# Performance work log

Hardware: AMD Instinct MI355X
Metric: run time of the kernel (lower is better)

## Reference

```python
import jax, jax.numpy as jnp
import numpy as np

B, S, E, H, V = 32, 128, 512, 512, 32000


def setup_inputs() -> dict:
    key = jax.random.key(0)
    ks = jax.random.split(key, 8)
    s_ih = 1.0 / np.sqrt(H)
    return {
        "embed_x": jax.random.normal(ks[0], (B, S, E), dtype=jnp.float32),
        "hidden": jax.random.normal(ks[1], (1, B, H), dtype=jnp.float32),
        "w_ih": jax.random.uniform(ks[2], (3 * H, E), dtype=jnp.float32, minval=-s_ih, maxval=s_ih),
        "w_hh": jax.random.uniform(ks[3], (3 * H, H), dtype=jnp.float32, minval=-s_ih, maxval=s_ih),
        "b_ih": jax.random.uniform(ks[4], (3 * H,), dtype=jnp.float32, minval=-s_ih, maxval=s_ih),
        "b_hh": jax.random.uniform(ks[5], (3 * H,), dtype=jnp.float32, minval=-s_ih, maxval=s_ih),
        "w_out": jax.random.normal(ks[6], (V, H), dtype=jnp.float32) * (1.0 / np.sqrt(H)),
    }


def reference(embed_x, hidden, w_ih, w_hh, b_ih, b_hh, w_out):
    # Single-layer GRU (PyTorch gate order: r, z, n), batch_first, then a
    # per-step bias-free projection to vocab. Dropout p=0 -> identity.
    h0 = hidden[0]                                  # [B, H]
    hsz = h0.shape[-1]
    # Precompute input contribution for all timesteps: [S, B, 3H]
    x_gates = jnp.einsum('bse,ge->sbg', embed_x, w_ih) + b_ih

    def step(h, xg):
        hg = h @ w_hh.T + b_hh                      # [B, 3H]
        xr, xz, xn = jnp.split(xg, 3, axis=-1)
        hr, hz, hn = jnp.split(hg, 3, axis=-1)
        r = jax.nn.sigmoid(xr + hr)
        z = jax.nn.sigmoid(xz + hz)
        n = jnp.tanh(xn + r * hn)
        h_new = (1.0 - z) * n + z * h
        return h_new, h_new

    _, hs = jax.lax.scan(step, h0, x_gates)         # hs: [S, B, H]
    # Projection to vocab (bias-free): [B, S, V]
    logits = jnp.einsum('sbh,vh->bsv', hs, w_out)
    return logits
```

## Files before the change

### kernel.cpp

```cpp
#include <hip/hip_runtime.h>

typedef unsigned short ushort_t;
typedef unsigned int uint_t;
typedef __attribute__((ext_vector_type(4))) float f32x4;
typedef __attribute__((ext_vector_type(8))) __bf16 bf16x8;

constexpr int BB = 32, SS = 128, EE = 512, HH = 512, VV = 32000;
constexpr int MM = BB * SS;
constexpr int G3 = 3 * HH;
constexpr int SCAN_WG = 32;

__device__ inline ushort_t f2b(float f) {
  union { float f; uint_t u; } v; v.f = f;
  uint_t r = v.u + 0x7fffu + ((v.u >> 16) & 1u);
  return (ushort_t)(r >> 16);
}
__device__ inline float b2f(ushort_t u) {
  union { float f; uint_t u; } v; v.u = ((uint_t)u) << 16;
  return v.f;
}

__global__ void cvt_bf16(const float* __restrict__ s, ushort_t* __restrict__ d, int n4) {
  int i = blockIdx.x * blockDim.x + threadIdx.x;
  if (i >= n4) return;
  float4 v = reinterpret_cast<const float4*>(s)[i];
  ushort4 o;
  o.x = f2b(v.x); o.y = f2b(v.y); o.z = f2b(v.z); o.w = f2b(v.w);
  reinterpret_cast<ushort4*>(d)[i] = o;
}

__global__ void cvt_split(const float* __restrict__ s, ushort_t* __restrict__ hi,
                          ushort_t* __restrict__ lo, int n4) {
  int i = blockIdx.x * blockDim.x + threadIdx.x;
  if (i >= n4) return;
  float4 v = reinterpret_cast<const float4*>(s)[i];
  float a[4] = {v.x, v.y, v.z, v.w};
  ushort4 oh, ol;
  ushort_t h;
  h = f2b(a[0]); oh.x = h; ol.x = f2b(a[0] - b2f(h));
  h = f2b(a[1]); oh.y = h; ol.y = f2b(a[1] - b2f(h));
  h = f2b(a[2]); oh.z = h; ol.z = f2b(a[2] - b2f(h));
  h = f2b(a[3]); oh.w = h; ol.w = f2b(a[3] - b2f(h));
  reinterpret_cast<ushort4*>(hi)[i] = oh;
  reinterpret_cast<ushort4*>(lo)[i] = ol;
}

__global__ __launch_bounds__(256) void gemm_bt(
    const ushort_t* __restrict__ A, const ushort_t* __restrict__ B,
    float* __restrict__ C, const float* __restrict__ bias,
    int M, int N, int K) {
  __shared__ alignas(16) ushort_t As[128 * 32];
  __shared__ alignas(16) ushort_t Bs[128 * 32];
  const int tid = threadIdx.x;
  const int wave = tid >> 6, lane = tid & 63;
  const int l16 = lane & 15, quad = lane >> 4;
  const int m0 = blockIdx.x * 128, n0 = blockIdx.y * 128;
  const int wm = (wave & 1) * 64, wn = (wave >> 1) * 64;

  f32x4 acc[4][4] = {};
  const int cbase = wave * 64 + lane;

  for (int kt = 0; kt < K; kt += 32) {
#pragma unroll
    for (int pass = 0; pass < 2; ++pass) {
      int c = cbase + pass * 256;
      int r = c >> 2;
      int kc = (c & 3) * 8;
      const ushort_t* ga = A + (size_t)(m0 + r) * K + kt + kc;
      const ushort_t* gb = B + (size_t)(n0 + r) * K + kt + kc;
      int ldsoff = (wave * 64 + pass * 256) * 16;
      __builtin_amdgcn_global_load_lds(
          (const __attribute__((address_space(1))) void*)ga,
          (__attribute__((address_space(3))) void*)((char*)As + ldsoff), 16, 0, 0);
      __builtin_amdgcn_global_load_lds(
          (const __attribute__((address_space(1))) void*)gb,
          (__attribute__((address_space(3))) void*)((char*)Bs + ldsoff), 16, 0, 0);
    }
    __syncthreads();
    bf16x8 af[4], bf[4];
#pragma unroll
    for (int i = 0; i < 4; ++i)
      af[i] = *(const bf16x8*)&As[(wm + i * 16 + l16) * 32 + quad * 8];
#pragma unroll
    for (int j = 0; j < 4; ++j)
      bf[j] = *(const bf16x8*)&Bs[(wn + j * 16 + l16) * 32 + quad * 8];
#pragma unroll
    for (int i = 0; i < 4; ++i)
#pragma unroll
      for (int j = 0; j < 4; ++j)
        acc[i][j] = __builtin_amdgcn_mfma_f32_16x16x32_bf16(af[i], bf[j], acc[i][j], 0, 0, 0);
    __syncthreads();
  }
#pragma unroll
  for (int i = 0; i < 4; ++i) {
    int row = m0 + wm + i * 16 + quad * 4;
#pragma unroll
    for (int j = 0; j < 4; ++j) {
      int col = n0 + wn + j * 16 + l16;
      float bv = bias ? bias[col] : 0.0f;
#pragma unroll
      for (int r = 0; r < 4; ++r)
        C[(size_t)(row + r) * N + col] = acc[i][j][r] + bv;
    }
  }
}

__global__ __launch_bounds__(256) void gru_scan(
    const float* __restrict__ xg,
    const float* __restrict__ h0,
    const float* __restrict__ b_hh,
    const ushort_t* __restrict__ whh_hi,
    const ushort_t* __restrict__ whh_lo,
    float* __restrict__ hf32,
    ushort_t* __restrict__ hbhi,
    ushort_t* __restrict__ hblo,
    ushort_t* __restrict__ hs,
    int* __restrict__ bar) {
  const int g = blockIdx.x;
  const int tid = threadIdx.x;
  const int wave = tid >> 6, lane = tid & 63;
  const int l16 = lane & 15, quad = lane >> 4;

  __shared__ alignas(16) ushort_t lds_whh_hi[48 * 512];
  __shared__ alignas(16) ushort_t lds_whh_lo[48 * 512];
  __shared__ float lds_part[4][3][32][17];

  for (int c = tid; c < 48 * 64; c += 256) {
    int lr = c >> 6;
    int kc = c & 63;
    int grow = (lr >> 4) * 512 + g * 16 + (lr & 15);
    const f32x4* srch = (const f32x4*)(whh_hi + (size_t)grow * 512 + kc * 8);
    const f32x4* srcl = (const f32x4*)(whh_lo + (size_t)grow * 512 + kc * 8);
    int db = lr * 1024 + ((kc * 16) ^ ((lr & 7) << 4));
    *(f32x4*)((char*)lds_whh_hi + db) = *srch;
    *(f32x4*)((char*)lds_whh_lo + db) = *srcl;
  }
  __syncthreads();

  const int gb = tid >> 3;
  const int jj = (tid & 7) * 2;
  const int gj = g * 16 + jj;
  const float bh_r0 = b_hh[gj],        bh_r1 = b_hh[gj + 1];
  const float bh_z0 = b_hh[512 + gj],  bh_z1 = b_hh[512 + gj + 1];
  const float bh_n0 = b_hh[1024 + gj], bh_n1 = b_hh[1024 + gj + 1];
  const float* xgp0 = xg + (size_t)gb * SS * G3 + gj;

  for (int t = 0; t < SS; ++t) {
    const int p = t & 1;

    const float* xgp = xgp0 + (size_t)t * G3;
    float2 fxr = *(const float2*)(xgp);
    float2 fxz = *(const float2*)(xgp + 512);
    float2 fxn = *(const float2*)(xgp + 1024);
    float2 fhv = (t == 0) ? *(const float2*)(h0 + gb * HH + gj)
                          : *(const float2*)(hf32 + p * (BB * HH) + gb * HH + gj);

    {
      const ushort_t* hhi = hbhi + p * (BB * HH);
      const ushort_t* hlo = hblo + p * (BB * HH);
      f32x4 acc[2][3] = {};
      const int kbase = wave * 128;
#pragma unroll
      for (int kk = 0; kk < 4; ++kk) {
        const int kw = kbase + kk * 32 + quad * 8;
        bf16x8 ah[2], al[2];
#pragma unroll
        for (int mt = 0; mt < 2; ++mt) {
          ah[mt] = *(const bf16x8*)(hhi + (size_t)(mt * 16 + l16) * HH + kw);
          al[mt] = *(const bf16x8*)(hlo + (size_t)(mt * 16 + l16) * HH + kw);
        }
        bf16x8 bh[3], bl[3];
#pragma unroll
        for (int nt = 0; nt < 3; ++nt) {
          int lr = nt * 16 + l16;
          int db = lr * 1024 + ((kw * 2) ^ ((lr & 7) << 4));
          bh[nt] = *(const bf16x8*)((const char*)lds_whh_hi + db);
          bl[nt] = *(const bf16x8*)((const char*)lds_whh_lo + db);
        }
#pragma unroll
        for (int mt = 0; mt < 2; ++mt)
#pragma unroll
          for (int nt = 0; nt < 3; ++nt) {
            acc[mt][nt] = __builtin_amdgcn_mfma_f32_16x16x32_bf16(ah[mt], bh[nt], acc[mt][nt], 0, 0, 0);
            acc[mt][nt] = __builtin_amdgcn_mfma_f32_16x16x32_bf16(ah[mt], bl[nt], acc[mt][nt], 0, 0, 0);
            acc[mt][nt] = __builtin_amdgcn_mfma_f32_16x16x32_bf16(al[mt], bh[nt], acc[mt][nt], 0, 0, 0);
          }
      }
#pragma unroll
      for (int mt = 0; mt < 2; ++mt)
#pragma unroll
        for (int nt = 0; nt < 3; ++nt)
#pragma unroll
          for (int r = 0; r < 4; ++r)
            lds_part[wave][nt][mt * 16 + quad * 4 + r][l16] = acc[mt][nt][r];
    }
    __syncthreads();

    {
      float xra[2] = {fxr.x, fxr.y};
      float xza[2] = {fxz.x, fxz.y};
      float xna[2] = {fxn.x, fxn.y};
      float hva[2] = {fhv.x, fhv.y};
      float bra[2] = {bh_r0, bh_r1};
      float bza[2] = {bh_z0, bh_z1};
      float bna[2] = {bh_n0, bh_n1};
      float outv[2]; ushort_t ohi[2], olo[2];
#pragma unroll
      for (int c = 0; c < 2; ++c) {
        int col = jj + c;
        float hr = lds_part[0][0][gb][col] + lds_part[1][0][gb][col]
                 + lds_part[2][0][gb][col] + lds_part[3][0][gb][col] + bra[c];
        float hz = lds_part[0][1][gb][col] + lds_part[1][1][gb][col]
                 + lds_part[2][1][gb][col] + lds_part[3][1][gb][col] + bza[c];
        float hn = lds_part[0][2][gb][col] + lds_part[1][2][gb][col]
                 + lds_part[2][2][gb][col] + lds_part[3][2][gb][col] + bna[c];
        float r = 1.f / (1.f + __expf(-(xra[c] + hr)));
        float z = 1.f / (1.f + __expf(-(xza[c] + hz)));
        float pre = xna[c] + r * hn;
        pre = fminf(fmaxf(pre, -15.f), 15.f);
        float e = __expf(2.f * pre);
        float n = (e - 1.f) / (e + 1.f);
        float hnew = (1.f - z) * n + z * hva[c];
        outv[c] = hnew;
        ushort_t hb = f2b(hnew);
        ohi[c] = hb;
        olo[c] = f2b(hnew - b2f(hb));
      }
      float* hf_next = hf32 + (p ^ 1) * (BB * HH);
      ushort_t* hhi_n = hbhi + (p ^ 1) * (BB * HH);
      ushort_t* hlo_n = hblo + (p ^ 1) * (BB * HH);
      *(float2*)(hf_next + gb * HH + gj) = make_float2(outv[0], outv[1]);
      ushort2 uh; uh.x = ohi[0]; uh.y = ohi[1];
      ushort2 ul; ul.x = olo[0]; ul.y = olo[1];
      *(ushort2*)(hhi_n + gb * HH + gj) = uh;
      *(ushort2*)(hlo_n + gb * HH + gj) = ul;
      *(ushort2*)(hs + (size_t)(gb * SS + t) * HH + gj) = uh;
    }

    __syncthreads();
    if (tid == 0) {
      __threadfence();
      atomicAdd(bar, 1);
      int target = (t + 1) * SCAN_WG;
      while (__hip_atomic_load(bar, __ATOMIC_RELAXED, __HIP_MEMORY_SCOPE_AGENT) < target)
        __builtin_amdgcn_s_sleep(2);
      __threadfence();
    }
    __syncthreads();
  }
}

extern "C" void kernel_launch(void* const* d_in, const int* in_sizes, int n_in,
                              void* d_out, int out_size, void* d_ws, size_t ws_size,
                              hipStream_t stream) {
  (void)in_sizes; (void)n_in; (void)out_size; (void)ws_size;
  const float* embed  = (const float*)d_in[0];
  const float* hidden = (const float*)d_in[1];
  const float* w_ih   = (const float*)d_in[2];
  const float* w_hh   = (const float*)d_in[3];
  const float* b_ih   = (const float*)d_in[4];
  const float* b_hh   = (const float*)d_in[5];
  const float* w_out  = (const float*)d_in[6];
  float* out = (float*)d_out;

  char* ws = (char*)d_ws;
  size_t off = 0;
  auto alloc = [&](size_t bytes) {
    void* p = ws + off;
    off += (bytes + 255) & ~(size_t)255;
    return p;
  };
  float*    xg     = (float*)   alloc((size_t)MM * G3 * 4);
  ushort_t* emb16  = (ushort_t*)alloc((size_t)MM * EE * 2);
  ushort_t* wih16  = (ushort_t*)alloc((size_t)G3 * EE * 2);
  ushort_t* whh_hi = (ushort_t*)alloc((size_t)G3 * HH * 2);
  ushort_t* whh_lo = (ushort_t*)alloc((size_t)G3 * HH * 2);
  ushort_t* wout16 = (ushort_t*)alloc((size_t)VV * HH * 2);
  ushort_t* hs16   = (ushort_t*)alloc((size_t)MM * HH * 2);
  float*    hf     = (float*)   alloc((size_t)2 * BB * HH * 4);
  ushort_t* hbhi   = (ushort_t*)alloc((size_t)2 * BB * HH * 2);
  ushort_t* hblo   = (ushort_t*)alloc((size_t)2 * BB * HH * 2);
  int*      bar    = (int*)     alloc(256);

  hipMemsetAsync(bar, 0, 256, stream);

  cvt_bf16 <<<2048,  256, 0, stream>>>(embed, emb16, MM * EE / 4);
  cvt_bf16 <<<768,   256, 0, stream>>>(w_ih, wih16, G3 * EE / 4);
  cvt_split<<<768,   256, 0, stream>>>(w_hh, whh_hi, whh_lo, G3 * HH / 4);
  cvt_bf16 <<<16000, 256, 0, stream>>>(w_out, wout16, VV * HH / 4);
  cvt_split<<<16,    256, 0, stream>>>(hidden, hbhi, hblo, BB * HH / 4);

  gemm_bt<<<dim3(MM / 128, G3 / 128), 256, 0, stream>>>(emb16, wih16, xg, b_ih, MM, G3, EE);

  gru_scan<<<SCAN_WG, 256, 0, stream>>>(xg, hidden, b_hh, whh_hi, whh_lo,
                                        hf, hbhi, hblo, hs16, bar);

  gemm_bt<<<dim3(MM / 128, VV / 128), 256, 0, stream>>>(hs16, wout16, out, nullptr, MM, VV, HH);
}
```

Before: 1.628 ms.

## Replace global grid barrier with per-slice counters and keep hidden state in registers

The single all-block barrier after each timestep is replaced by per-wave waits on a counter covering the eight blocks that produce that wave's 128-column K-slice, so each wave waits only for the data it consumes. Blocks increment their group counter without a trailing spin. Each thread now keeps its own fp32 hidden values in registers, dropping the fp32 hidden buffer and its global reads and writes. h is read and written through relaxed agent-scope atomics with no explicit fences, which risks ordering and visibility problems.

```diff
diff --git a/kernel.cpp b/kernel.cpp
--- a/kernel.cpp
+++ b/kernel.cpp
@@ -111,7 +111,6 @@
     const float* __restrict__ b_hh,
     const ushort_t* __restrict__ whh_hi,
     const ushort_t* __restrict__ whh_lo,
-    float* __restrict__ hf32,
     ushort_t* __restrict__ hbhi,
     ushort_t* __restrict__ hblo,
     ushort_t* __restrict__ hs,
@@ -144,6 +143,12 @@
   const float bh_z0 = b_hh[512 + gj],  bh_z1 = b_hh[512 + gj + 1];
   const float bh_n0 = b_hh[1024 + gj], bh_n1 = b_hh[1024 + gj + 1];
   const float* xgp0 = xg + (size_t)gb * SS * G3 + gj;
+  float hv0 = h0[gb * HH + gj], hv1 = h0[gb * HH + gj + 1];
+
+  int* const barq   = bar + wave * 16;
+  int* const bar_pr = bar + (g >> 3) * 16;
+
+  union U16B { unsigned long long q[2]; bf16x8 v; };
 
   for (int t = 0; t < SS; ++t) {
     const int p = t & 1;
@@ -152,23 +157,42 @@
     float2 fxr = *(const float2*)(xgp);
     float2 fxz = *(const float2*)(xgp + 512);
     float2 fxn = *(const float2*)(xgp + 1024);
-    float2 fhv = (t == 0) ? *(const float2*)(h0 + gb * HH + gj)
-                          : *(const float2*)(hf32 + p * (BB * HH) + gb * HH + gj);
+
+    if (lane == 0) {
+      int target = t * 8;
+      while (__hip_atomic_load(barq, __ATOMIC_RELAXED, __HIP_MEMORY_SCOPE_AGENT) < target)
+        __builtin_amdgcn_s_sleep(1);
+    }
+    asm volatile("" ::: "memory");
+
+    const ushort_t* hhi = hbhi + p * (BB * HH);
+    const ushort_t* hlo = hblo + p * (BB * HH);
+    const int kbase = wave * 128;
+    bf16x8 ah[2][4], al[2][4];
+#pragma unroll
+    for (int kk = 0; kk < 4; ++kk) {
+      const int kw = kbase + kk * 32 + quad * 8;
+#pragma unroll
+      for (int mt = 0; mt < 2; ++mt) {
+        const unsigned long long* ph =
+            (const unsigned long long*)(hhi + (size_t)(mt * 16 + l16) * HH + kw);
+        const unsigned long long* pl =
+            (const unsigned long long*)(hlo + (size_t)(mt * 16 + l16) * HH + kw);
+        U16B th, tl;
+        th.q[0] = __hip_atomic_load(ph,     __ATOMIC_RELAXED, __HIP_MEMORY_SCOPE_AGENT);
+        th.q[1] = __hip_atomic_load(ph + 1, __ATOMIC_RELAXED, __HIP_MEMORY_SCOPE_AGENT);
+        tl.q[0] = __hip_atomic_load(pl,     __ATOMIC_RELAXED, __HIP_MEMORY_SCOPE_AGENT);
+        tl.q[1] = __hip_atomic_load(pl + 1, __ATOMIC_RELAXED, __HIP_MEMORY_SCOPE_AGENT);
+        ah[mt][kk] = th.v;
+        al[mt][kk] = tl.v;
+      }
+    }
 
     {
-      const ushort_t* hhi = hbhi + p * (BB * HH);
-      const ushort_t* hlo = hblo + p * (BB * HH);
       f32x4 acc[2][3] = {};
-      const int kbase = wave * 128;
 #pragma unroll
       for (int kk = 0; kk < 4; ++kk) {
         const int kw = kbase + kk * 32 + quad * 8;
-        bf16x8 ah[2], al[2];
-#pragma unroll
-        for (int mt = 0; mt < 2; ++mt) {
-          ah[mt] = *(const bf16x8*)(hhi + (size_t)(mt * 16 + l16) * HH + kw);
-          al[mt] = *(const bf16x8*)(hlo + (size_t)(mt * 16 + l16) * HH + kw);
-        }
         bf16x8 bh[3], bl[3];
 #pragma unroll
         for (int nt = 0; nt < 3; ++nt) {
@@ -181,9 +205,9 @@
         for (int mt = 0; mt < 2; ++mt)
 #pragma unroll
           for (int nt = 0; nt < 3; ++nt) {
-            acc[mt][nt] = __builtin_amdgcn_mfma_f32_16x16x32_bf16(ah[mt], bh[nt], acc[mt][nt], 0, 0, 0);
-            acc[mt][nt] = __builtin_amdgcn_mfma_f32_16x16x32_bf16(ah[mt], bl[nt], acc[mt][nt], 0, 0, 0);
-            acc[mt][nt] = __builtin_amdgcn_mfma_f32_16x16x32_bf16(al[mt], bh[nt], acc[mt][nt], 0, 0, 0);
+            acc[mt][nt] = __builtin_amdgcn_mfma_f32_16x16x32_bf16(ah[mt][kk], bh[nt], acc[mt][nt], 0, 0, 0);
+            acc[mt][nt] = __builtin_amdgcn_mfma_f32_16x16x32_bf16(ah[mt][kk], bl[nt], acc[mt][nt], 0, 0, 0);
+            acc[mt][nt] = __builtin_amdgcn_mfma_f32_16x16x32_bf16(al[mt][kk], bh[nt], acc[mt][nt], 0, 0, 0);
           }
       }
 #pragma unroll
@@ -200,7 +224,7 @@
       float xra[2] = {fxr.x, fxr.y};
       float xza[2] = {fxz.x, fxz.y};
       float xna[2] = {fxn.x, fxn.y};
-      float hva[2] = {fhv.x, fhv.y};
+      float hva[2] = {hv0, hv1};
       float bra[2] = {bh_r0, bh_r1};
       float bza[2] = {bh_z0, bh_z1};
       float bna[2] = {bh_n0, bh_n1};
@@ -226,27 +250,22 @@
         ohi[c] = hb;
         olo[c] = f2b(hnew - b2f(hb));
       }
-      float* hf_next = hf32 + (p ^ 1) * (BB * HH);
+      hv0 = outv[0]; hv1 = outv[1];
       ushort_t* hhi_n = hbhi + (p ^ 1) * (BB * HH);
       ushort_t* hlo_n = hblo + (p ^ 1) * (BB * HH);
-      *(float2*)(hf_next + gb * HH + gj) = make_float2(outv[0], outv[1]);
-      ushort2 uh; uh.x = ohi[0]; uh.y = ohi[1];
-      ushort2 ul; ul.x = olo[0]; ul.y = olo[1];
-      *(ushort2*)(hhi_n + gb * HH + gj) = uh;
-      *(ushort2*)(hlo_n + gb * HH + gj) = ul;
-      *(ushort2*)(hs + (size_t)(gb * SS + t) * HH + gj) = uh;
+      uint_t uh = (uint_t)ohi[0] | ((uint_t)ohi[1] << 16);
+      uint_t ul = (uint_t)olo[0] | ((uint_t)olo[1] << 16);
+      __hip_atomic_store((uint_t*)(hhi_n + gb * HH + gj), uh,
+                         __ATOMIC_RELAXED, __HIP_MEMORY_SCOPE_AGENT);
+      __hip_atomic_store((uint_t*)(hlo_n + gb * HH + gj), ul,
+                         __ATOMIC_RELAXED, __HIP_MEMORY_SCOPE_AGENT);
+      ushort2 uh2; uh2.x = ohi[0]; uh2.y = ohi[1];
+      *(ushort2*)(hs + (size_t)(gb * SS + t) * HH + gj) = uh2;
     }
 
     __syncthreads();
-    if (tid == 0) {
-      __threadfence();
-      atomicAdd(bar, 1);
-      int target = (t + 1) * SCAN_WG;
-      while (__hip_atomic_load(bar, __ATOMIC_RELAXED, __HIP_MEMORY_SCOPE_AGENT) < target)
-        __builtin_amdgcn_s_sleep(2);
-      __threadfence();
-    }
-    __syncthreads();
+    if (tid == 0)
+      __hip_atomic_fetch_add(bar_pr, 1, __ATOMIC_RELAXED, __HIP_MEMORY_SCOPE_AGENT);
   }
 }
 
@@ -277,7 +296,6 @@
   ushort_t* whh_lo = (ushort_t*)alloc((size_t)G3 * HH * 2);
   ushort_t* wout16 = (ushort_t*)alloc((size_t)VV * HH * 2);
   ushort_t* hs16   = (ushort_t*)alloc((size_t)MM * HH * 2);
-  float*    hf     = (float*)   alloc((size_t)2 * BB * HH * 4);
   ushort_t* hbhi   = (ushort_t*)alloc((size_t)2 * BB * HH * 2);
   ushort_t* hblo   = (ushort_t*)alloc((size_t)2 * BB * HH * 2);
   int*      bar    = (int*)     alloc(256);
@@ -293,7 +311,7 @@
   gemm_bt<<<dim3(MM / 128, G3 / 128), 256, 0, stream>>>(emb16, wih16, xg, b_ih, MM, G3, EE);
 
   gru_scan<<<SCAN_WG, 256, 0, stream>>>(xg, hidden, b_hh, whh_hi, whh_lo,
-                                        hf, hbhi, hblo, hs16, bar);
+                                        hbhi, hblo, hs16, bar);
 
   gemm_bt<<<dim3(MM / 128, VV / 128), 256, 0, stream>>>(hs16, wout16, out, nullptr, MM, VV, HH);
 }
```

Result: faster. 1.513 ms (-7.0%).
